# Kernel optimization log

Measured on AMD Instinct MI355X. Metric: run time of the kernel, lower is better.

## Reference

```python
import jax, jax.numpy as jnp
import numpy as np

B, N, D, H = 4, 2048, 256, 8
DH = D // H

def setup_inputs() -> dict:
    key = jax.random.key(0)
    ks = jax.random.split(key, 7)
    s = 1.0 / np.sqrt(DH)
    return {
        "sequences": jax.random.normal(ks[0], (B, N, D), dtype=jnp.float32),
        "Wq": jax.random.uniform(ks[1], (H, DH, DH), jnp.float32, -s, s),
        "bq": jax.random.uniform(ks[2], (H, DH), jnp.float32, -s, s),
        "Wk": jax.random.uniform(ks[3], (H, DH, DH), jnp.float32, -s, s),
        "bk": jax.random.uniform(ks[4], (H, DH), jnp.float32, -s, s),
        "Wv": jax.random.uniform(ks[5], (H, DH, DH), jnp.float32, -s, s),
        "bv": jax.random.uniform(ks[6], (H, DH), jnp.float32, -s, s),
    }

def reference(sequences, Wq, bq, Wk, bk, Wv, bv):
    # sequences: [B, N, D] -> [B, N, H, DH] (head h sees columns h*DH:(h+1)*DH)
    x = sequences.reshape(B, N, H, DH)
    # per-head Linear: y = x @ W.T + b
    q = jnp.einsum("bnhd,hed->bnhe", x, Wq) + bq
    k = jnp.einsum("bnhd,hed->bnhe", x, Wk) + bk
    v = jnp.einsum("bnhd,hed->bnhe", x, Wv) + bv
    scores = jnp.einsum("bnhe,bmhe->bhnm", q, k) / jnp.sqrt(jnp.float32(DH))
    attn = jax.nn.softmax(scores, axis=-1)  # [B, H, N, N]
    out = jnp.einsum("bhnm,bmhe->bnhe", attn, v)
    # hstack of per-head results == concat over last dim == reshape
    return out.reshape(B, N, D)
```

## Files before the change

### kernel.cpp

```cpp
#include <hip/hip_runtime.h>
#include <hip/hip_bf16.h>

typedef __bf16 bf16;
typedef __bf16 bf16x8 __attribute__((ext_vector_type(8)));
typedef __bf16 bf16x4 __attribute__((ext_vector_type(4)));
typedef float  f32x4  __attribute__((ext_vector_type(4)));

#define B_  4
#define N_  2048
#define D_  256
#define H_  8
#define DH_ 32
#define QKV_ELEMS (B_*H_*N_*DH_)

#define QSC    (0.17677669529663687f * 1.4426950408889634f)
#define NBIAS  (-17.312340490667562f)

#if __has_builtin(__builtin_amdgcn_exp2f)
__device__ inline float exp2_hw(float x) { return __builtin_amdgcn_exp2f(x); }
#else
__device__ inline float exp2_hw(float x) {
    float r; asm volatile("v_exp_f32 %0, %1" : "=v"(r) : "v"(x)); return r;
}
#endif

__device__ inline void gload_lds16(const bf16* g, bf16* l) {
    __builtin_amdgcn_global_load_lds(
        (const __attribute__((address_space(1))) void*)g,
        (__attribute__((address_space(3))) void*)l, 16, 0, 0);
}

__device__ inline bf16x8 ldcvt8(const float* __restrict__ p) {
    f32x4 a = *(const f32x4*)p;
    f32x4 b = *(const f32x4*)(p + 4);
    bf16x8 r;
    r[0] = (bf16)a[0]; r[1] = (bf16)a[1]; r[2] = (bf16)a[2]; r[3] = (bf16)a[3];
    r[4] = (bf16)b[0]; r[5] = (bf16)b[1]; r[6] = (bf16)b[2]; r[7] = (bf16)b[3];
    return r;
}

__global__ __launch_bounds__(256, 4) void qkv_proj_kernel(
    const float* __restrict__ x,
    const float* __restrict__ Wq, const float* __restrict__ bq,
    const float* __restrict__ Wk, const float* __restrict__ bk,
    const float* __restrict__ Wv, const float* __restrict__ bv,
    bf16* __restrict__ Qg, bf16* __restrict__ Kg, bf16* __restrict__ Vg)
{
    const int bh = blockIdx.x & 31, nt = blockIdx.x >> 5;
    const int h  = bh & (H_-1),    b  = bh >> 3;
    const int wave = threadIdx.x >> 6, lane = threadIdx.x & 63;
    const int l16 = lane & 15, q4 = lane >> 4;
    const int n0 = nt*64 + wave*16;

    bf16x8 wqf[2], wkf[2], wvf[2];
    f32x4  bq4[2], bk4[2];
    float  bvs[2];
    #pragma unroll
    for (int half = 0; half < 2; ++half) {
        wqf[half] = ldcvt8(Wq + (h*DH_ + half*16 + l16)*DH_ + q4*8);
        wkf[half] = ldcvt8(Wk + (h*DH_ + half*16 + l16)*DH_ + q4*8);
        wvf[half] = ldcvt8(Wv + (h*DH_ + half*16 + l16)*DH_ + q4*8);
        bq4[half] = *(const f32x4*)(bq + h*DH_ + half*16 + q4*4);
        bk4[half] = *(const f32x4*)(bk + h*DH_ + half*16 + q4*4);
        bvs[half] = bv[h*DH_ + half*16 + l16];
    }

    bf16x8 xf = ldcvt8(x + ((size_t)(b*N_ + n0 + l16))*D_ + h*DH_ + q4*8);
    const f32x4 z = {0.f,0.f,0.f,0.f};

    #pragma unroll
    for (int half = 0; half < 2; ++half) {
        f32x4 dq = __builtin_amdgcn_mfma_f32_16x16x32_bf16(wqf[half], xf, z, 0, 0, 0);
        f32x4 dk = __builtin_amdgcn_mfma_f32_16x16x32_bf16(wkf[half], xf, z, 0, 0, 0);
        f32x4 dv = __builtin_amdgcn_mfma_f32_16x16x32_bf16(xf, wvf[half], z, 0, 0, 0);
        bf16x4 pq, pk, pv;
        #pragma unroll
        for (int r = 0; r < 4; ++r) {
            pq[r] = (bf16)((dq[r] + bq4[half][r]) * QSC);
            pk[r] = (bf16)(dk[r] + bk4[half][r]);
            pv[r] = (bf16)(dv[r] + bvs[half]);
        }
        const size_t row = ((size_t)bh*N_ + n0 + l16)*DH_ + half*16 + q4*4;
        *(bf16x4*)(Qg + row) = pq;
        *(bf16x4*)(Kg + row) = pk;
        const int e = half*16 + l16;
        const size_t idx = ((size_t)bh << 16) + ((size_t)(n0 >> 5) << 10)
                         + (e << 5) + (q4 << 3) + (((n0 >> 4) & 1) << 2);
        *(bf16x4*)(Vg + idx) = pv;
    }
}

__global__ __launch_bounds__(256, 4) void attn_kernel(
    const bf16* __restrict__ Qg, const bf16* __restrict__ Kg,
    const bf16* __restrict__ Vg, float* __restrict__ out)
{
    const int bh = blockIdx.x & 31;
    const int qt = blockIdx.x >> 5;
    const int h  = bh & (H_-1), b = bh >> 3;
    const int lane = threadIdx.x & 63;
    const int wave = threadIdx.x >> 6;
    const int l16 = lane & 15, q4 = lane >> 4;

    __shared__ bf16 Kl[2][128*DH_];
    __shared__ bf16 Vl[2][128*DH_];

    const bf16* Kb = Kg + (size_t)bh*N_*DH_;
    const bf16* Vb = Vg + ((size_t)bh << 16);
    const int qrow0 = qt*64 + wave*16;

    bf16x8 qb = *(const bf16x8*)(Qg + ((size_t)bh*N_ + qrow0 + l16)*DH_ + q4*8);

    f32x4 ot0 = {0,0,0,0}, ot1 = {0,0,0,0};
    float rs = 0.f;
    const f32x4 zb = {NBIAS, NBIAS, NBIAS, NBIAS};

    const int seg = wave*1024 + lane*8;

    gload_lds16(Kb + seg,       &Kl[0][wave*1024]);
    gload_lds16(Kb + seg + 512, &Kl[0][wave*1024 + 512]);
    gload_lds16(Vb + seg,       &Vl[0][wave*1024]);
    gload_lds16(Vb + seg + 512, &Vl[0][wave*1024 + 512]);
    __syncthreads();

    for (int kt = 0; kt < 16; ++kt) {
        const int cur = kt & 1, nxt = cur ^ 1, nkt = (kt + 1) & 15;

        const bf16* gk = Kb + (size_t)nkt*4096 + seg;
        const bf16* gv = Vb + (size_t)nkt*4096 + seg;
        gload_lds16(gk,       &Kl[nxt][wave*1024]);
        gload_lds16(gk + 512, &Kl[nxt][wave*1024 + 512]);
        gload_lds16(gv,       &Vl[nxt][wave*1024]);
        gload_lds16(gv + 512, &Vl[nxt][wave*1024 + 512]);

        #pragma unroll
        for (int hh = 0; hh < 2; ++hh) {
            f32x4 st4[4];
            #pragma unroll
            for (int kc = 0; kc < 4; ++kc) {
                bf16x8 kf = *(const bf16x8*)(&Kl[cur][(hh*64 + kc*16 + l16)*DH_ + q4*8]);
                st4[kc] = __builtin_amdgcn_mfma_f32_16x16x32_bf16(kf, qb, zb, 0, 0, 0);
            }
            #pragma unroll
            for (int kk = 0; kk < 2; ++kk) {
                bf16x8 pb;
                #pragma unroll
                for (int hf = 0; hf < 2; ++hf)
                    #pragma unroll
                    for (int r = 0; r < 4; ++r) {
                        const float p = exp2_hw(st4[kk*2 + hf][r]);
                        rs += p;
                        pb[hf*4 + r] = (bf16)p;
                    }
                const int g = hh*2 + kk;
                bf16x8 v0 = *(const bf16x8*)(&Vl[cur][g*1024 + l16*DH_ + q4*8]);
                bf16x8 v1 = *(const bf16x8*)(&Vl[cur][g*1024 + (16 + l16)*DH_ + q4*8]);
                ot0 = __builtin_amdgcn_mfma_f32_16x16x32_bf16(v0, pb, ot0, 0, 0, 0);
                ot1 = __builtin_amdgcn_mfma_f32_16x16x32_bf16(v1, pb, ot1, 0, 0, 0);
            }
        }

        __syncthreads();
    }

    rs += __shfl_xor(rs, 16);
    rs += __shfl_xor(rs, 32);
    const float inv = 1.0f / rs;

    #pragma unroll
    for (int dhh = 0; dhh < 2; ++dhh) {
        const f32x4& o = dhh ? ot1 : ot0;
        f32x4 w;
        #pragma unroll
        for (int r = 0; r < 4; ++r) w[r] = o[r] * inv;
        *(f32x4*)(out + ((size_t)b*N_ + qrow0 + l16)*D_ + h*DH_ + dhh*16 + q4*4) = w;
    }
}

extern "C" void kernel_launch(void* const* d_in, const int* in_sizes, int n_in,
                              void* d_out, int out_size, void* d_ws, size_t ws_size,
                              hipStream_t stream)
{
    const float* x  = (const float*)d_in[0];
    const float* Wq = (const float*)d_in[1];
    const float* bq = (const float*)d_in[2];
    const float* Wk = (const float*)d_in[3];
    const float* bk = (const float*)d_in[4];
    const float* Wv = (const float*)d_in[5];
    const float* bv = (const float*)d_in[6];
    float* out = (float*)d_out;

    bf16* Qg = (bf16*)d_ws;
    bf16* Kg = Qg + QKV_ELEMS;
    bf16* Vg = Kg + QKV_ELEMS;

    qkv_proj_kernel<<<dim3(B_*H_*32), dim3(256), 0, stream>>>(
        x, Wq, bq, Wk, bk, Wv, bv, Qg, Kg, Vg);
    attn_kernel<<<dim3(B_*H_*(N_/64)), dim3(256), 0, stream>>>(Qg, Kg, Vg, out);
}
```

Baseline: 105.8 us.

## Split attention keys across two blocks and add combine kernel

The attention kernel now uses 512-thread blocks covering 128 query rows, and each block processes only half of the key sequence (split-K). Partial unnormalized outputs and row sums go to fp32 workspace, and a new combine kernel adds the two halves and normalizes. This works because a fixed bias replaces a running max, so the partial sums can simply be added. It is meant to give each block more queries sharing every K/V tile load and to shorten the serial loop, at the cost of extra workspace traffic and a third kernel launch.

Measured after the change: 107.0 us. About the same (+1.1%).

```diff
diff --git a/kernel.cpp b/kernel.cpp
--- a/kernel.cpp
+++ b/kernel.cpp
@@ -90,15 +90,16 @@
     }
 }
 
-__global__ __launch_bounds__(256, 4) void attn_kernel(
+__global__ __launch_bounds__(512, 8) void attn_kernel(
     const bf16* __restrict__ Qg, const bf16* __restrict__ Kg,
-    const bf16* __restrict__ Vg, float* __restrict__ out)
+    const bf16* __restrict__ Vg, float* __restrict__ Pws, float* __restrict__ Rws)
 {
     const int bh = blockIdx.x & 31;
-    const int qt = blockIdx.x >> 5;
-    const int h  = bh & (H_-1), b = bh >> 3;
-    const int lane = threadIdx.x & 63;
-    const int wave = threadIdx.x >> 6;
+    const int qk = blockIdx.x >> 5;
+    const int ks = qk & 1, qt = qk >> 1;
+    const int t    = threadIdx.x;
+    const int lane = t & 63;
+    const int wave = t >> 6;
     const int l16 = lane & 15, q4 = lane >> 4;
 
     __shared__ bf16 Kl[2][128*DH_];
@@ -106,7 +107,8 @@
 
     const bf16* Kb = Kg + (size_t)bh*N_*DH_;
     const bf16* Vb = Vg + ((size_t)bh << 16);
-    const int qrow0 = qt*64 + wave*16;
+    const int qrow0 = qt*128 + wave*16;
+    const int kt0   = ks*8;
 
     bf16x8 qb = *(const bf16x8*)(Qg + ((size_t)bh*N_ + qrow0 + l16)*DH_ + q4*8);
 
@@ -114,23 +116,18 @@
     float rs = 0.f;
     const f32x4 zb = {NBIAS, NBIAS, NBIAS, NBIAS};
 
-    const int seg = wave*1024 + lane*8;
-
-    gload_lds16(Kb + seg,       &Kl[0][wave*1024]);
-    gload_lds16(Kb + seg + 512, &Kl[0][wave*1024 + 512]);
-    gload_lds16(Vb + seg,       &Vl[0][wave*1024]);
-    gload_lds16(Vb + seg + 512, &Vl[0][wave*1024 + 512]);
+    const int seg = wave*512 + lane*8;
+
+    gload_lds16(Kb + (size_t)kt0*4096 + seg, &Kl[0][seg]);
+    gload_lds16(Vb + (size_t)kt0*4096 + seg, &Vl[0][seg]);
     __syncthreads();
 
-    for (int kt = 0; kt < 16; ++kt) {
-        const int cur = kt & 1, nxt = cur ^ 1, nkt = (kt + 1) & 15;
-
-        const bf16* gk = Kb + (size_t)nkt*4096 + seg;
-        const bf16* gv = Vb + (size_t)nkt*4096 + seg;
-        gload_lds16(gk,       &Kl[nxt][wave*1024]);
-        gload_lds16(gk + 512, &Kl[nxt][wave*1024 + 512]);
-        gload_lds16(gv,       &Vl[nxt][wave*1024]);
-        gload_lds16(gv + 512, &Vl[nxt][wave*1024 + 512]);
+    for (int i = 0; i < 8; ++i) {
+        const int cur = i & 1, nxt = cur ^ 1;
+        const int nt = (kt0 + i + 1) & 15;
+
+        gload_lds16(Kb + (size_t)nt*4096 + seg, &Kl[nxt][seg]);
+        gload_lds16(Vb + (size_t)nt*4096 + seg, &Vl[nxt][seg]);
 
         #pragma unroll
         for (int hh = 0; hh < 2; ++hh) {
@@ -164,16 +161,34 @@
 
     rs += __shfl_xor(rs, 16);
     rs += __shfl_xor(rs, 32);
-    const float inv = 1.0f / rs;
-
+
+    float* po = Pws + (((size_t)(ks*32 + bh))*N_ + qrow0 + l16)*DH_;
+    *(f32x4*)(po + q4*4)      = ot0;
+    *(f32x4*)(po + 16 + q4*4) = ot1;
+    if (q4 == 0)
+        Rws[((size_t)(ks*32 + bh))*N_ + qrow0 + l16] = rs;
+}
+
+__global__ __launch_bounds__(256, 8) void combine_kernel(
+    const float* __restrict__ Pws, const float* __restrict__ Rws,
+    float* __restrict__ out)
+{
+    const int flat = blockIdx.x*256 + threadIdx.x;
+    const int e4 = flat << 2;
+    const int bh = e4 >> 16;
+    const int rem = e4 & 65535;
+    const int n = rem >> 5, d4 = rem & 31;
+    const int b = bh >> 3, h = bh & 7;
+
+    const size_t i0 = ((size_t)bh*N_ + n)*DH_ + d4;
+    const size_t i1 = ((size_t)(32 + bh)*N_ + n)*DH_ + d4;
+    f32x4 s0 = *(const f32x4*)(Pws + i0);
+    f32x4 s1 = *(const f32x4*)(Pws + i1);
+    const float inv = 1.0f / (Rws[(size_t)bh*N_ + n] + Rws[(size_t)(32 + bh)*N_ + n]);
+    f32x4 w;
     #pragma unroll
-    for (int dhh = 0; dhh < 2; ++dhh) {
-        const f32x4& o = dhh ? ot1 : ot0;
-        f32x4 w;
-        #pragma unroll
-        for (int r = 0; r < 4; ++r) w[r] = o[r] * inv;
-        *(f32x4*)(out + ((size_t)b*N_ + qrow0 + l16)*D_ + h*DH_ + dhh*16 + q4*4) = w;
-    }
+    for (int r = 0; r < 4; ++r) w[r] = (s0[r] + s1[r]) * inv;
+    *(f32x4*)(out + ((size_t)b*N_ + n)*D_ + h*DH_ + d4) = w;
 }
 
 extern "C" void kernel_launch(void* const* d_in, const int* in_sizes, int n_in,
@@ -189,11 +204,14 @@
     const float* bv = (const float*)d_in[6];
     float* out = (float*)d_out;
 
-    bf16* Qg = (bf16*)d_ws;
-    bf16* Kg = Qg + QKV_ELEMS;
-    bf16* Vg = Kg + QKV_ELEMS;
+    bf16*  Qg  = (bf16*)d_ws;
+    bf16*  Kg  = Qg + QKV_ELEMS;
+    bf16*  Vg  = Kg + QKV_ELEMS;
+    float* Pws = (float*)(Vg + QKV_ELEMS);
+    float* Rws = Pws + 2*QKV_ELEMS;
 
     qkv_proj_kernel<<<dim3(B_*H_*32), dim3(256), 0, stream>>>(
         x, Wq, bq, Wk, bk, Wv, bv, Qg, Kg, Vg);
-    attn_kernel<<<dim3(B_*H_*(N_/64)), dim3(256), 0, stream>>>(Qg, Kg, Vg, out);
-}
+    attn_kernel<<<dim3(B_*H_*32), dim3(512), 0, stream>>>(Qg, Kg, Vg, Pws, Rws);
+    combine_kernel<<<dim3(2048), dim3(256), 0, stream>>>(Pws, Rws, out);
+}
```
